# Kernel optimization log

Hardware: AMD Instinct MI355X
Metric: run time of the kernel (lower is better)

The kernel has to match this reference:

```python
import jax, jax.numpy as jnp
import numpy as np

L = 2999          # sequence length (odd -> clean consider_pad branch)
D = 512           # hidden dim
NB = 16           # number of gaussian basis functions
PENALTY = 0.1
SIGMAS = np.array([0.1, 0.5], dtype=np.float32)
INV_SQRT_2PI = 1.0 / np.sqrt(2.0 * np.pi)


def _gaussian(x, mu, sigma):
    z = (x - mu) / sigma
    return INV_SQRT_2PI / sigma * jnp.exp(-0.5 * z * z)


def _make_basis():
    # torch.meshgrid(linspace(0,1,NB//len(sigmas)), sigmas) with 'ij' indexing, flattened
    base_mu = np.linspace(0.0, 1.0, NB // len(SIGMAS)).astype(np.float32)
    mus = np.repeat(base_mu, len(SIGMAS))          # (NB,)
    sigs = np.tile(SIGMAS, NB // len(SIGMAS))      # (NB,)
    return jnp.asarray(mus), jnp.asarray(sigs)


def _make_G(basis_mu, basis_sigma):
    # get_positions with consider_pad=True, odd L: positions over padded interval
    shift = 1.0 / L
    pos = jnp.linspace(-0.5 + shift, 1.5 - shift, 2 * L - 1)          # (P,)
    F = _gaussian(pos[None, :], basis_mu[:, None], basis_sigma[:, None])  # (NB, P)
    I = jnp.eye(NB, dtype=jnp.float32)
    G_full = F.T @ jnp.linalg.inv(F @ F.T + PENALTY * I)              # (P, NB)
    half = (L - 1) // 2
    return G_full[half:-half]                                          # (L, NB)


def setup_inputs() -> dict:
    key = jax.random.key(0)
    k1, k2, k3, k4 = jax.random.split(key, 4)
    B = 32
    query = jax.random.normal(k1, (B, 1, D), dtype=jnp.float32)
    keys = jax.random.normal(k2, (B, L, D), dtype=jnp.float32)
    values = jax.random.normal(k3, (B, L, D), dtype=jnp.float32)
    mask = jnp.ones((B, L), dtype=bool)
    W_enc = jax.random.normal(k4, (D, D), dtype=jnp.float32) / np.sqrt(D)
    basis_mu, basis_sigma = _make_basis()
    G = _make_G(basis_mu, basis_sigma)
    return {"query": query, "keys": keys, "values": values, "mask": mask,
            "W_enc": W_enc, "G": G, "basis_mu": basis_mu, "basis_sigma": basis_sigma}


def reference(query, keys, values, mask, W_enc, G, basis_mu, basis_sigma):
    # --- encoder: discrete bilinear attention -> disc_p, mu, variance ---
    q = query[:, 0, :]                                   # (B, D)
    scores = jnp.einsum('bld,de,be->bl', keys, W_enc, q) / jnp.sqrt(jnp.float32(D))
    scores = jnp.where(mask, scores, -jnp.inf)
    disc_p = jax.nn.softmax(scores, axis=-1)             # (B, L)
    # discrete positions (consider_pad=False branch): midpoints of [0,1]
    pshift = 1.0 / (2.0 * L)
    pos = jnp.linspace(pshift, 1.0 - pshift, L)          # (L,)
    mu = disc_p @ pos                                    # (B,)
    e2 = disc_p @ (pos * pos)
    variance = jnp.clip(e2 - mu * mu, 1e-7, None)
    sigma_sq = jnp.clip(variance, 1e-12, None)           # softmax: sigma_sq = variance
    # --- continuous softmax: r_j = E_{N(mu,sigma_sq)}[psi_j] = N(mu; mu_j, sigma_sq+sig_j^2)
    tot_var = sigma_sq[:, None] + basis_sigma[None, :] ** 2      # (B, NB)
    r = INV_SQRT_2PI / jnp.sqrt(tot_var) * jnp.exp(
        -0.5 * (mu[:, None] - basis_mu[None, :]) ** 2 / tot_var)  # (B, NB)
    # --- value function: B = values^T G (all sequences full length -> shared G)
    Bmat = jnp.einsum('bld,ln->bdn', values, G)          # (B, D, NB)
    c = jnp.einsum('bdn,bn->bd', Bmat, r)[:, None, :]    # (B, 1, D)
    return c
```

## Files before the change

kernel.cpp:

```cpp
#include <hip/hip_runtime.h>
#include <math.h>

#define LL 2999
#define DD 512
#define NBASIS 16
#define BB 32
#define NCH 64

static constexpr float INV_SQRT_2PI = 0.3989422804014327f;
static constexpr float INV_SQRT_D   = 0.044194173824159216f;

__global__ __launch_bounds__(256) void k_gemv_t(const float* __restrict__ q,
                                                const float* __restrict__ W,
                                                float* __restrict__ t) {
    int wid  = blockIdx.x * 4 + (threadIdx.x >> 6);
    int lane = threadIdx.x & 63;
    int b = wid >> 9;
    int d = wid & 511;
    const float4* wrow = (const float4*)(W + (size_t)d * DD);
    const float4* qrow = (const float4*)(q + (size_t)b * DD);
    float sum = 0.f;
    #pragma unroll
    for (int e = lane; e < DD / 4; e += 64) {
        float4 wv = wrow[e], qv = qrow[e];
        sum += wv.x * qv.x + wv.y * qv.y + wv.z * qv.z + wv.w * qv.w;
    }
    #pragma unroll
    for (int off = 32; off > 0; off >>= 1) sum += __shfl_xor(sum, off);
    if (lane == 0) t[(size_t)b * DD + d] = sum;
}

__global__ __launch_bounds__(256) void k_scores(const float* __restrict__ keys,
                                                const float* __restrict__ t,
                                                float* __restrict__ scores) {
    int wid = blockIdx.x * 4 + (threadIdx.x >> 6);
    if (wid >= BB * LL) return;
    int lane = threadIdx.x & 63;
    int b = wid / LL;
    const float4* krow = (const float4*)(keys + (size_t)wid * DD);
    const float4* trow = (const float4*)(t + (size_t)b * DD);
    float sum = 0.f;
    #pragma unroll
    for (int e = lane; e < DD / 4; e += 64) {
        float4 kv = krow[e], tv = trow[e];
        sum += kv.x * tv.x + kv.y * tv.y + kv.z * tv.z + kv.w * tv.w;
    }
    #pragma unroll
    for (int off = 32; off > 0; off >>= 1) sum += __shfl_xor(sum, off);
    if (lane == 0) scores[wid] = sum * INV_SQRT_D;
}

__global__ __launch_bounds__(256) void k_stats(const float* __restrict__ scores,
                                               const float* __restrict__ bmu,
                                               const float* __restrict__ bsig,
                                               float* __restrict__ r) {
    __shared__ float sh[256];
    int b = blockIdx.x, t = threadIdx.x;
    const float* srow = scores + (size_t)b * LL;

    float loc[12];
    float mx = -INFINITY;
    #pragma unroll
    for (int i = 0; i < 12; ++i) {
        int l = t + i * 256;
        if (l < LL) { loc[i] = srow[l]; mx = fmaxf(mx, loc[i]); }
    }
    sh[t] = mx; __syncthreads();
    for (int s = 128; s > 0; s >>= 1) { if (t < s) sh[t] = fmaxf(sh[t], sh[t + s]); __syncthreads(); }
    mx = sh[0]; __syncthreads();

    const float pshift = 1.0f / (2.0f * LL);
    const float step   = (1.0f - 2.0f * pshift) / (LL - 1);
    float s0 = 0.f, s1 = 0.f, s2 = 0.f;
    #pragma unroll
    for (int i = 0; i < 12; ++i) {
        int l = t + i * 256;
        if (l < LL) {
            float e = expf(loc[i] - mx);
            float p = pshift + l * step;
            s0 += e; s1 += e * p; s2 += e * p * p;
        }
    }
    sh[t] = s0; __syncthreads();
    for (int s = 128; s > 0; s >>= 1) { if (t < s) sh[t] += sh[t + s]; __syncthreads(); }
    s0 = sh[0]; __syncthreads();
    sh[t] = s1; __syncthreads();
    for (int s = 128; s > 0; s >>= 1) { if (t < s) sh[t] += sh[t + s]; __syncthreads(); }
    s1 = sh[0]; __syncthreads();
    sh[t] = s2; __syncthreads();
    for (int s = 128; s > 0; s >>= 1) { if (t < s) sh[t] += sh[t + s]; __syncthreads(); }
    s2 = sh[0]; __syncthreads();

    if (t < NBASIS) {
        float mu  = s1 / s0;
        float e2  = s2 / s0;
        float var = fmaxf(e2 - mu * mu, 1e-7f);
        float sg  = bsig[t];
        float tv  = var + sg * sg;
        float dm  = mu - bmu[t];
        r[b * NBASIS + t] = INV_SQRT_2PI / sqrtf(tv) * expf(-0.5f * dm * dm / tv);
    }
}

__global__ __launch_bounds__(256) void k_w(const float* __restrict__ G,
                                           const float* __restrict__ r,
                                           float* __restrict__ w) {
    int idx = blockIdx.x * 256 + threadIdx.x;
    if (idx >= BB * LL) return;
    int b = idx / LL;
    int l = idx - b * LL;
    const float4* gr = (const float4*)(G + (size_t)l * NBASIS);
    const float4* rr = (const float4*)(r + (size_t)b * NBASIS);
    float sum = 0.f;
    #pragma unroll
    for (int i = 0; i < 4; ++i) {
        float4 g = gr[i], rv = rr[i];
        sum += g.x * rv.x + g.y * rv.y + g.z * rv.z + g.w * rv.w;
    }
    w[idx] = sum;
}

__global__ __launch_bounds__(128) void k_partial(const float* __restrict__ values,
                                                 const float* __restrict__ w,
                                                 float* __restrict__ part) {
    int b  = blockIdx.x / NCH;
    int ch = blockIdx.x % NCH;
    int t  = threadIdx.x;
    const int Lc = (LL + NCH - 1) / NCH;
    int l0 = ch * Lc;
    int l1 = l0 + Lc; if (l1 > LL) l1 = LL;
    const float* wrow = w + (size_t)b * LL;
    float4 acc = make_float4(0.f, 0.f, 0.f, 0.f);
    for (int l = l0; l < l1; ++l) {
        float wv = wrow[l];
        float4 vv = ((const float4*)(values + ((size_t)b * LL + l) * DD))[t];
        acc.x += vv.x * wv; acc.y += vv.y * wv; acc.z += vv.z * wv; acc.w += vv.w * wv;
    }
    ((float4*)(part + (size_t)blockIdx.x * DD))[t] = acc;
}

__global__ __launch_bounds__(256) void k_reduce(const float* __restrict__ part,
                                                float* __restrict__ out) {
    int idx = blockIdx.x * 256 + threadIdx.x;
    int b = idx >> 9;
    int d = idx & 511;
    const float* p = part + (size_t)b * NCH * DD + d;
    float sum = 0.f;
    #pragma unroll 8
    for (int ch = 0; ch < NCH; ++ch) sum += p[(size_t)ch * DD];
    out[idx] = sum;
}

extern "C" void kernel_launch(void* const* d_in, const int* in_sizes, int n_in,
                              void* d_out, int out_size, void* d_ws, size_t ws_size,
                              hipStream_t stream) {
    const float* query  = (const float*)d_in[0];
    const float* keys   = (const float*)d_in[1];
    const float* values = (const float*)d_in[2];
    const float* W_enc  = (const float*)d_in[4];
    const float* G      = (const float*)d_in[5];
    const float* bmu    = (const float*)d_in[6];
    const float* bsig   = (const float*)d_in[7];
    float* out = (float*)d_out;
    float* ws  = (float*)d_ws;

    float* t_buf  = ws;
    float* scores = ws + 16384;
    float* r_buf  = ws + 112352;
    float* w_buf  = ws + 112864;
    float* part   = ws + 208832;

    k_gemv_t<<<(BB * DD) / 4, 256, 0, stream>>>(query, W_enc, t_buf);
    k_scores<<<(BB * LL + 3) / 4, 256, 0, stream>>>(keys, t_buf, scores);
    k_stats<<<BB, 256, 0, stream>>>(scores, bmu, bsig, r_buf);
    k_w<<<(BB * LL + 255) / 256, 256, 0, stream>>>(G, r_buf, w_buf);
    k_partial<<<BB * NCH, 128, 0, stream>>>(values, w_buf, part);
    k_reduce<<<(BB * DD + 255) / 256, 256, 0, stream>>>(part, out);
}
```

Before: 89.89 us.

## Reassociate value projection through G to stream keys and values concurrently

The value path now computes values^T G (B x D x NB) per chunk, which no longer depends on the softmax statistics. That lets the keys-scores pass and the values pass run inside one launch as two disjoint sets of blocks. A final per-batch kernel computes the softmax moments and r, then contracts the partial Bmat with r. This removes the serial dependency between the two large reads and cuts the launch count from six to three, in exchange for 16x more FLOPs and partial-buffer traffic on the values side. Only 256 blocks handle values, with 375 rows each, so load balance and latency of the value blocks may limit the gain.

```diff
diff --git a/kernel.cpp b/kernel.cpp
--- a/kernel.cpp
+++ b/kernel.cpp
@@ -5,7 +5,11 @@
 #define DD 512
 #define NBASIS 16
 #define BB 32
-#define NCH 64
+
+#define NCHV 8
+#define LCV 375
+#define NSBLK 768
+#define NTHR 256
 
 static constexpr float INV_SQRT_2PI = 0.3989422804014327f;
 static constexpr float INV_SQRT_D   = 0.044194173824159216f;
@@ -30,125 +34,128 @@
     if (lane == 0) t[(size_t)b * DD + d] = sum;
 }
 
-__global__ __launch_bounds__(256) void k_scores(const float* __restrict__ keys,
-                                                const float* __restrict__ t,
-                                                float* __restrict__ scores) {
-    int wid = blockIdx.x * 4 + (threadIdx.x >> 6);
-    if (wid >= BB * LL) return;
-    int lane = threadIdx.x & 63;
-    int b = wid / LL;
-    const float4* krow = (const float4*)(keys + (size_t)wid * DD);
-    const float4* trow = (const float4*)(t + (size_t)b * DD);
-    float sum = 0.f;
-    #pragma unroll
-    for (int e = lane; e < DD / 4; e += 64) {
-        float4 kv = krow[e], tv = trow[e];
-        sum += kv.x * tv.x + kv.y * tv.y + kv.z * tv.z + kv.w * tv.w;
+__global__ __launch_bounds__(NTHR) void k_stream(
+    const float* __restrict__ keys, const float* __restrict__ values,
+    const float* __restrict__ G, const float* __restrict__ t_buf,
+    float* __restrict__ scores, float* __restrict__ part)
+{
+    __shared__ float sh[LCV * NBASIS];
+    const int bid = blockIdx.x, tid = threadIdx.x;
+
+    if (bid < BB * NCHV) {
+        int b  = bid >> 3;
+        int ch = bid & (NCHV - 1);
+        int l0 = ch * LCV;
+        int l1 = l0 + LCV; if (l1 > LL) l1 = LL;
+        int cnt = (l1 - l0) * NBASIS;
+        for (int i = tid; i < cnt; i += NTHR) sh[i] = G[(size_t)l0 * NBASIS + i];
+        __syncthreads();
+
+        float accx[NBASIS], accy[NBASIS];
+        #pragma unroll
+        for (int n = 0; n < NBASIS; ++n) { accx[n] = 0.f; accy[n] = 0.f; }
+        const float* vb = values + (size_t)b * LL * DD + 2 * tid;
+        for (int l = l0; l < l1; ++l) {
+            float2 vv = *(const float2*)(vb + (size_t)l * DD);
+            const float* g = sh + (l - l0) * NBASIS;
+            #pragma unroll
+            for (int n = 0; n < NBASIS; ++n) {
+                float gn = g[n];
+                accx[n] += vv.x * gn;
+                accy[n] += vv.y * gn;
+            }
+        }
+        #pragma unroll
+        for (int n = 0; n < NBASIS; ++n) {
+            float2* pp = (float2*)(part + ((size_t)bid * NBASIS + n) * DD);
+            pp[tid] = make_float2(accx[n], accy[n]);
+        }
+    } else {
+        int wave = tid >> 6, lane = tid & 63;
+        int swave = (bid - BB * NCHV) * 4 + wave;
+        for (int row = swave; row < BB * LL; row += NSBLK * 4) {
+            int b = row / LL;
+            const float4* krow = (const float4*)(keys + (size_t)row * DD);
+            const float4* trow = (const float4*)(t_buf + (size_t)b * DD);
+            float s = 0.f;
+            #pragma unroll
+            for (int e = lane; e < DD / 4; e += 64) {
+                float4 kv = krow[e], tv = trow[e];
+                s += kv.x * tv.x + kv.y * tv.y + kv.z * tv.z + kv.w * tv.w;
+            }
+            #pragma unroll
+            for (int off = 32; off > 0; off >>= 1) s += __shfl_xor(s, off);
+            if (lane == 0) scores[row] = s * INV_SQRT_D;
+        }
     }
-    #pragma unroll
-    for (int off = 32; off > 0; off >>= 1) sum += __shfl_xor(sum, off);
-    if (lane == 0) scores[wid] = sum * INV_SQRT_D;
 }
 
-__global__ __launch_bounds__(256) void k_stats(const float* __restrict__ scores,
-                                               const float* __restrict__ bmu,
-                                               const float* __restrict__ bsig,
-                                               float* __restrict__ r) {
-    __shared__ float sh[256];
-    int b = blockIdx.x, t = threadIdx.x;
+__global__ __launch_bounds__(512) void k_finish(
+    const float* __restrict__ scores, const float* __restrict__ part,
+    const float* __restrict__ bmu, const float* __restrict__ bsig,
+    float* __restrict__ out)
+{
+    __shared__ float sh[512];
+    __shared__ float shr[NBASIS];
+    int b = blockIdx.x, tid = threadIdx.x;
     const float* srow = scores + (size_t)b * LL;
 
-    float loc[12];
+    float loc[6];
     float mx = -INFINITY;
     #pragma unroll
-    for (int i = 0; i < 12; ++i) {
-        int l = t + i * 256;
+    for (int i = 0; i < 6; ++i) {
+        int l = tid + i * 512;
         if (l < LL) { loc[i] = srow[l]; mx = fmaxf(mx, loc[i]); }
     }
-    sh[t] = mx; __syncthreads();
-    for (int s = 128; s > 0; s >>= 1) { if (t < s) sh[t] = fmaxf(sh[t], sh[t + s]); __syncthreads(); }
+    sh[tid] = mx; __syncthreads();
+    for (int s = 256; s > 0; s >>= 1) { if (tid < s) sh[tid] = fmaxf(sh[tid], sh[tid + s]); __syncthreads(); }
     mx = sh[0]; __syncthreads();
 
     const float pshift = 1.0f / (2.0f * LL);
     const float step   = (1.0f - 2.0f * pshift) / (LL - 1);
     float s0 = 0.f, s1 = 0.f, s2 = 0.f;
     #pragma unroll
-    for (int i = 0; i < 12; ++i) {
-        int l = t + i * 256;
+    for (int i = 0; i < 6; ++i) {
+        int l = tid + i * 512;
         if (l < LL) {
             float e = expf(loc[i] - mx);
             float p = pshift + l * step;
             s0 += e; s1 += e * p; s2 += e * p * p;
         }
     }
-    sh[t] = s0; __syncthreads();
-    for (int s = 128; s > 0; s >>= 1) { if (t < s) sh[t] += sh[t + s]; __syncthreads(); }
+    sh[tid] = s0; __syncthreads();
+    for (int s = 256; s > 0; s >>= 1) { if (tid < s) sh[tid] += sh[tid + s]; __syncthreads(); }
     s0 = sh[0]; __syncthreads();
-    sh[t] = s1; __syncthreads();
-    for (int s = 128; s > 0; s >>= 1) { if (t < s) sh[t] += sh[t + s]; __syncthreads(); }
+    sh[tid] = s1; __syncthreads();
+    for (int s = 256; s > 0; s >>= 1) { if (tid < s) sh[tid] += sh[tid + s]; __syncthreads(); }
     s1 = sh[0]; __syncthreads();
-    sh[t] = s2; __syncthreads();
-    for (int s = 128; s > 0; s >>= 1) { if (t < s) sh[t] += sh[t + s]; __syncthreads(); }
+    sh[tid] = s2; __syncthreads();
+    for (int s = 256; s > 0; s >>= 1) { if (tid < s) sh[tid] += sh[tid + s]; __syncthreads(); }
     s2 = sh[0]; __syncthreads();
 
-    if (t < NBASIS) {
+    if (tid < NBASIS) {
         float mu  = s1 / s0;
         float e2  = s2 / s0;
         float var = fmaxf(e2 - mu * mu, 1e-7f);
-        float sg  = bsig[t];
+        float sg  = bsig[tid];
         float tv  = var + sg * sg;
-        float dm  = mu - bmu[t];
-        r[b * NBASIS + t] = INV_SQRT_2PI / sqrtf(tv) * expf(-0.5f * dm * dm / tv);
+        float dm  = mu - bmu[tid];
+        shr[tid] = INV_SQRT_2PI / sqrtf(tv) * expf(-0.5f * dm * dm / tv);
     }
-}
+    __syncthreads();
 
-__global__ __launch_bounds__(256) void k_w(const float* __restrict__ G,
-                                           const float* __restrict__ r,
-                                           float* __restrict__ w) {
-    int idx = blockIdx.x * 256 + threadIdx.x;
-    if (idx >= BB * LL) return;
-    int b = idx / LL;
-    int l = idx - b * LL;
-    const float4* gr = (const float4*)(G + (size_t)l * NBASIS);
-    const float4* rr = (const float4*)(r + (size_t)b * NBASIS);
+    float rl[NBASIS];
+    #pragma unroll
+    for (int n = 0; n < NBASIS; ++n) rl[n] = shr[n];
+    int d = tid;
     float sum = 0.f;
     #pragma unroll
-    for (int i = 0; i < 4; ++i) {
-        float4 g = gr[i], rv = rr[i];
-        sum += g.x * rv.x + g.y * rv.y + g.z * rv.z + g.w * rv.w;
+    for (int ch = 0; ch < NCHV; ++ch) {
+        const float* pp = part + ((size_t)(b * NCHV + ch) * NBASIS) * DD + d;
+        #pragma unroll
+        for (int n = 0; n < NBASIS; ++n) sum += pp[(size_t)n * DD] * rl[n];
     }
-    w[idx] = sum;
-}
-
-__global__ __launch_bounds__(128) void k_partial(const float* __restrict__ values,
-                                                 const float* __restrict__ w,
-                                                 float* __restrict__ part) {
-    int b  = blockIdx.x / NCH;
-    int ch = blockIdx.x % NCH;
-    int t  = threadIdx.x;
-    const int Lc = (LL + NCH - 1) / NCH;
-    int l0 = ch * Lc;
-    int l1 = l0 + Lc; if (l1 > LL) l1 = LL;
-    const float* wrow = w + (size_t)b * LL;
-    float4 acc = make_float4(0.f, 0.f, 0.f, 0.f);
-    for (int l = l0; l < l1; ++l) {
-        float wv = wrow[l];
-        float4 vv = ((const float4*)(values + ((size_t)b * LL + l) * DD))[t];
-        acc.x += vv.x * wv; acc.y += vv.y * wv; acc.z += vv.z * wv; acc.w += vv.w * wv;
-    }
-    ((float4*)(part + (size_t)blockIdx.x * DD))[t] = acc;
-}
-
-__global__ __launch_bounds__(256) void k_reduce(const float* __restrict__ part,
-                                                float* __restrict__ out) {
-    int idx = blockIdx.x * 256 + threadIdx.x;
-    int b = idx >> 9;
-    int d = idx & 511;
-    const float* p = part + (size_t)b * NCH * DD + d;
-    float sum = 0.f;
-    #pragma unroll 8
-    for (int ch = 0; ch < NCH; ++ch) sum += p[(size_t)ch * DD];
-    out[idx] = sum;
+    out[(size_t)b * DD + d] = sum;
 }
 
 extern "C" void kernel_launch(void* const* d_in, const int* in_sizes, int n_in,
@@ -166,14 +173,10 @@
 
     float* t_buf  = ws;
     float* scores = ws + 16384;
-    float* r_buf  = ws + 112352;
-    float* w_buf  = ws + 112864;
-    float* part   = ws + 208832;
+    float* part   = ws + 112352;
 
     k_gemv_t<<<(BB * DD) / 4, 256, 0, stream>>>(query, W_enc, t_buf);
-    k_scores<<<(BB * LL + 3) / 4, 256, 0, stream>>>(keys, t_buf, scores);
-    k_stats<<<BB, 256, 0, stream>>>(scores, bmu, bsig, r_buf);
-    k_w<<<(BB * LL + 255) / 256, 256, 0, stream>>>(G, r_buf, w_buf);
-    k_partial<<<BB * NCH, 128, 0, stream>>>(values, w_buf, part);
-    k_reduce<<<(BB * DD + 255) / 256, 256, 0, stream>>>(part, out);
+    k_stream<<<BB * NCHV + NSBLK, NTHR, 0, stream>>>(keys, values, G, t_buf,
+                                                     scores, part);
+    k_finish<<<BB, 512, 0, stream>>>(scores, part, bmu, bsig, out);
 }
```

New measurement: 137.4 us. 1.53x slower.
